# Performance work log

Hardware: AMD Instinct MI355X
Metric: run time of the kernel (lower is better)

The kernel has to match this reference:

```python
import jax, jax.numpy as jnp
import numpy as np


def setup_inputs() -> dict:
    key = jax.random.key(0)
    ks = jax.random.split(key, 5)
    B, Lq, Lkv, HQ, H, D, S, BS = 1, 256, 4096, 32, 2, 128, 16, 64
    q = jax.random.normal(ks[0], (B, Lq, HQ, D), jnp.float32)
    k = jax.random.normal(ks[1], (B, Lkv, H, D), jnp.float32)
    v = jax.random.normal(ks[2], (B, Lkv, H, D), jnp.float32)
    w = jax.random.uniform(ks[3], (B, Lq, HQ, S), jnp.float32)
    block_indices = jax.random.randint(ks[4], (B, Lq, H, S), 0, Lkv // BS).astype(jnp.int32)
    return {"q": q, "k": k, "v": v, "w": w, "block_indices": block_indices, "block_size": BS}


def reference(q, k, v, w, block_indices, block_size):
    # q: (B, Lq, HQ, D); k,v: (B, Lkv, H, D); w: (B, Lq, HQ, num_weights);
    # block_indices: (B, Lq, H, S) int32, entries < 0 are skipped.
    B, Lq, HQ, D = q.shape
    H = k.shape[2]
    S = block_indices.shape[-1]
    G = HQ // H  # query heads per kv head
    nb = k.shape[1] // block_size
    sm_scale = 1.0 / (D ** 0.5)  # default scale in the kernel

    # Reshape KV into blocks: (B, H, nb, BS, D)
    kb = k.reshape(B, nb, block_size, H, D).transpose(0, 3, 1, 2, 4)
    vb = v.reshape(B, nb, block_size, H, D).transpose(0, 3, 1, 2, 4)

    idx = block_indices.transpose(0, 2, 1, 3)  # (B, H, Lq, S)
    valid = idx >= 0
    idx = jnp.maximum(idx, 0)

    # Gather selected blocks per (batch, kv_head): -> (B, H, Lq, S, BS, D)
    gather = jax.vmap(jax.vmap(lambda blocks, ind: blocks[ind]))
    kg = gather(kb, idx)
    vg = gather(vb, idx)

    # Group query heads by kv head: (B, H, Lq, G, D)
    qh = q.reshape(B, Lq, H, G, D).transpose(0, 2, 1, 3, 4)

    # Per-block scores and per-block softmax over the BS keys (axis u)
    scores = jnp.einsum('bhlgd,bhlsud->bhlgsu', qh, kg) * sm_scale
    p = jax.nn.softmax(scores, axis=-1)

    # Per-(head, block) learned weight; only first S weights of w are used.
    wh = w[..., :S].reshape(B, Lq, H, G, S).transpose(0, 2, 1, 3, 4)  # (B,H,Lq,G,S)
    coef = wh * valid[:, :, :, None, :].astype(p.dtype)
    p = p * coef[..., None]

    o = jnp.einsum('bhlgsu,bhlsud->bhlgd', p, vg)  # (B, H, Lq, G, D)
    return o.transpose(0, 2, 1, 3, 4).reshape(B, Lq, HQ, D)
```

## Files before the change

kernel.cpp:

```cpp
#include <hip/hip_runtime.h>
#include <hip/hip_bf16.h>


namespace {

constexpr int kLq = 256, kHQ = 32, kH = 2, kG = 16, kD = 128, kS = 16;
constexpr int kNB = 64;
constexpr float kScaleLog2e = 0.08838834764831845f * 1.4426950408889634f;

constexpr int kKPackN = kH * kNB * 16 * 64;
constexpr int kPStr   = 72;
constexpr int kSStr   = 136;

constexpr int kQOff = 0;
constexpr int kPOff = 32768;

typedef short s16x8 __attribute__((ext_vector_type(8)));
typedef float f32x4 __attribute__((ext_vector_type(4)));

union U32BF2 { unsigned int u; __hip_bfloat162 h; };
union FragU  { uint4 u; s16x8 v; };

static __device__ inline unsigned int pk_bf16(float a, float b) {
    U32BF2 z; z.h = __float22bfloat162_rn(make_float2(a, b));
    return z.u;
}

__global__ __launch_bounds__(256)
void pack_kv(const float* __restrict__ k, const float* __restrict__ v,
             uint4* __restrict__ kp, uint4* __restrict__ vp)
{
    __shared__ unsigned short S_s[32 * kSStr];

    const int bid  = blockIdx.x;
    const int isV  = bid & 1;
    const int half = (bid >> 1) & 1;
    const int blk  = (bid >> 2) & 63;
    const int h    = bid >> 8;
    const int t    = threadIdx.x;
    const int lane = t & 63, n = lane & 15, quad = lane >> 4;
    const int wv   = t >> 6;

    {
        const float* src = (isV ? v : k) +
            ((size_t)(blk * 64 + half * 32) * kH + h) * kD;
        const int r0 = t >> 5, c4 = (t & 31) << 2;
        #pragma unroll
        for (int p = 0; p < 4; ++p) {
            const int r = p * 8 + r0;
            const float4 f = *(const float4*)(src + (size_t)r * (kH * kD) + c4);
            *(unsigned int*)&S_s[r * kSStr + c4]     = pk_bf16(f.x, f.y);
            *(unsigned int*)&S_s[r * kSStr + c4 + 2] = pk_bf16(f.z, f.w);
        }
    }
    __syncthreads();

    const size_t obase = (size_t)(h * 64 + blk) * 16 * 64;
    if (!isV) {
        #pragma unroll
        for (int rep = 0; rep < 2; ++rep) {
            const int cl    = wv * 2 + rep;
            const int t_loc = cl >> 2, st = cl & 3;
            const int c     = (2 * half + t_loc) * 4 + st;
            const int u_loc = t_loc * 16 + n;
            kp[obase + (size_t)c * 64 + lane] =
                *(const uint4*)&S_s[u_loc * kSStr + st * 32 + quad * 8];
        }
    } else {
        #pragma unroll
        for (int rep = 0; rep < 2; ++rep) {
            const int dt = wv * 2 + rep;
            const int c  = dt * 2 + half;
            const int d  = dt * 16 + n;
            unsigned short s[8];
            #pragma unroll
            for (int j = 0; j < 8; ++j) s[j] = S_s[(quad * 8 + j) * kSStr + d];
            uint4 val;
            val.x = s[0] | ((unsigned)s[1] << 16);
            val.y = s[2] | ((unsigned)s[3] << 16);
            val.z = s[4] | ((unsigned)s[5] << 16);
            val.w = s[6] | ((unsigned)s[7] << 16);
            vp[obase + (size_t)c * 64 + lane] = val;
        }
    }
}

__global__ __launch_bounds__(512, 4)
void hsa_main(const float* __restrict__ q, const float* __restrict__ w,
              const int* __restrict__ bidx, const uint4* __restrict__ kp,
              const uint4* __restrict__ vp, float* __restrict__ out)
{
    __shared__ __align__(16) unsigned char smem[69632];

    const int bid  = blockIdx.x;
    const int l    = bid >> 1;
    const int h    = bid & 1;
    const int tid  = threadIdx.x;
    const int wave = tid >> 6;
    const int lane = tid & 63;
    const int n    = lane & 15;
    const int quad = lane >> 4;

    unsigned char* qlds = smem + kQOff + wave * 4096 + lane * 16;
    {
        const float* qb = q + ((size_t)l * kHQ + h * kG + n) * kD + quad * 8;
        #pragma unroll
        for (int st = 0; st < 4; ++st) {
            const float4 f0 = *(const float4*)(qb + st * 32);
            const float4 f1 = *(const float4*)(qb + st * 32 + 4);
            uint4 z;
            z.x = pk_bf16(f0.x, f0.y); z.y = pk_bf16(f0.z, f0.w);
            z.z = pk_bf16(f1.x, f1.y); z.w = pk_bf16(f1.z, f1.w);
            *(uint4*)(qlds + st * 1024) = z;
        }
    }

    int   baseA, baseB;
    float wvalA, wvalB;
    {
        const int sA = wave * 2, sB = wave * 2 + 1;
        const int biA = bidx[(size_t)(l * kH + h) * kS + sA];
        const int biB = bidx[(size_t)(l * kH + h) * kS + sB];
        wvalA = (biA < 0) ? 0.f : w[((size_t)l * kHQ + h * kG + n) * kS + sA];
        wvalB = (biB < 0) ? 0.f : w[((size_t)l * kHQ + h * kG + n) * kS + sB];
        baseA = (h * kNB + max(biA, 0)) * 1024;
        baseB = (h * kNB + max(biB, 0)) * 1024;
    }

    unsigned short* PA = (unsigned short*)(smem + kPOff + wave * 4608);
    unsigned short* PB = PA + kG * kPStr;

    FragU kA[4], kB[4], vrA[4], vrB[4];
    #pragma unroll
    for (int st = 0; st < 4; ++st) kA[st].u = kp[baseA + st * 64 + lane];
    #pragma unroll
    for (int st = 0; st < 4; ++st) kB[st].u = kp[baseB + st * 64 + lane];
    #pragma unroll
    for (int i = 0; i < 4; ++i)    vrA[i].u = vp[baseA + i * 64 + lane];
    #pragma unroll
    for (int i = 0; i < 4; ++i)    vrB[i].u = vp[baseA + (4 + i) * 64 + lane];
    __builtin_amdgcn_sched_barrier(0);

    f32x4 oacc[8];
    #pragma unroll
    for (int dt = 0; dt < 8; ++dt) oacc[dt] = (f32x4){0.f, 0.f, 0.f, 0.f};

    float partA = 0.f, partB = 0.f;
    #pragma unroll
    for (int t = 0; t < 4; ++t) {
        {
            f32x4 sc = {0.f, 0.f, 0.f, 0.f};
            #pragma unroll
            for (int st = 0; st < 4; ++st) {
                const s16x8 aq = *(const s16x8*)(qlds + st * 1024);
                sc = __builtin_amdgcn_mfma_f32_16x16x32_bf16(kA[st].v, aq, sc, 0, 0, 0);
            }
            if (t < 3) {
                #pragma unroll
                for (int st = 0; st < 4; ++st)
                    kA[st].u = kp[baseA + ((t + 1) * 4 + st) * 64 + lane];
            }
            __builtin_amdgcn_sched_barrier(0);
            #pragma unroll
            for (int r = 0; r < 4; ++r) {
                sc[r] = exp2f(sc[r] * kScaleLog2e);
                partA += sc[r];
            }
            const unsigned long long pq =
                ((unsigned long long)pk_bf16(sc[2], sc[3]) << 32) | pk_bf16(sc[0], sc[1]);
            *(unsigned long long*)&PA[n * kPStr + t * 16 + quad * 4] = pq;
        }
        {
            f32x4 sc = {0.f, 0.f, 0.f, 0.f};
            #pragma unroll
            for (int st = 0; st < 4; ++st) {
                const s16x8 aq = *(const s16x8*)(qlds + st * 1024);
                sc = __builtin_amdgcn_mfma_f32_16x16x32_bf16(kB[st].v, aq, sc, 0, 0, 0);
            }
            if (t < 3) {
                #pragma unroll
                for (int st = 0; st < 4; ++st)
                    kB[st].u = kp[baseB + ((t + 1) * 4 + st) * 64 + lane];
            }
            __builtin_amdgcn_sched_barrier(0);
            #pragma unroll
            for (int r = 0; r < 4; ++r) {
                sc[r] = exp2f(sc[r] * kScaleLog2e);
                partB += sc[r];
            }
            const unsigned long long pq =
                ((unsigned long long)pk_bf16(sc[2], sc[3]) << 32) | pk_bf16(sc[0], sc[1]);
            *(unsigned long long*)&PB[n * kPStr + t * 16 + quad * 4] = pq;
        }
    }

    partA += __shfl_xor(partA, 16);
    partA += __shfl_xor(partA, 32);
    partB += __shfl_xor(partB, 16);
    partB += __shfl_xor(partB, 32);
    const float coefA = wvalA / partA;
    const float coefB = wvalB / partB;

    const f32x4 zero = {0.f, 0.f, 0.f, 0.f};

    {
        const s16x8 bf0 = *(const s16x8*)&PA[n * kPStr + quad * 8];
        const s16x8 bf1 = *(const s16x8*)&PA[n * kPStr + 32 + quad * 8];

        {
            f32x4 p0 = __builtin_amdgcn_mfma_f32_16x16x32_bf16(vrA[0].v, bf0, zero, 0, 0, 0);
            p0       = __builtin_amdgcn_mfma_f32_16x16x32_bf16(vrA[1].v, bf1, p0,   0, 0, 0);
            f32x4 p1 = __builtin_amdgcn_mfma_f32_16x16x32_bf16(vrA[2].v, bf0, zero, 0, 0, 0);
            p1       = __builtin_amdgcn_mfma_f32_16x16x32_bf16(vrA[3].v, bf1, p1,   0, 0, 0);
            #pragma unroll
            for (int i = 0; i < 4; ++i) vrA[i].u = vp[baseA + (8 + i) * 64 + lane];
            __builtin_amdgcn_sched_barrier(0);
            #pragma unroll
            for (int r = 0; r < 4; ++r) {
                oacc[0][r] = fmaf(coefA, p0[r], oacc[0][r]);
                oacc[1][r] = fmaf(coefA, p1[r], oacc[1][r]);
            }
        }
        {
            f32x4 p0 = __builtin_amdgcn_mfma_f32_16x16x32_bf16(vrB[0].v, bf0, zero, 0, 0, 0);
            p0       = __builtin_amdgcn_mfma_f32_16x16x32_bf16(vrB[1].v, bf1, p0,   0, 0, 0);
            f32x4 p1 = __builtin_amdgcn_mfma_f32_16x16x32_bf16(vrB[2].v, bf0, zero, 0, 0, 0);
            p1       = __builtin_amdgcn_mfma_f32_16x16x32_bf16(vrB[3].v, bf1, p1,   0, 0, 0);
            #pragma unroll
            for (int i = 0; i < 4; ++i) vrB[i].u = vp[baseA + (12 + i) * 64 + lane];
            __builtin_amdgcn_sched_barrier(0);
            #pragma unroll
            for (int r = 0; r < 4; ++r) {
                oacc[2][r] = fmaf(coefA, p0[r], oacc[2][r]);
                oacc[3][r] = fmaf(coefA, p1[r], oacc[3][r]);
            }
        }
        {
            f32x4 p0 = __builtin_amdgcn_mfma_f32_16x16x32_bf16(vrA[0].v, bf0, zero, 0, 0, 0);
            p0       = __builtin_amdgcn_mfma_f32_16x16x32_bf16(vrA[1].v, bf1, p0,   0, 0, 0);
            f32x4 p1 = __builtin_amdgcn_mfma_f32_16x16x32_bf16(vrA[2].v, bf0, zero, 0, 0, 0);
            p1       = __builtin_amdgcn_mfma_f32_16x16x32_bf16(vrA[3].v, bf1, p1,   0, 0, 0);
            #pragma unroll
            for (int i = 0; i < 4; ++i) vrA[i].u = vp[baseB + i * 64 + lane];
            __builtin_amdgcn_sched_barrier(0);
            #pragma unroll
            for (int r = 0; r < 4; ++r) {
                oacc[4][r] = fmaf(coefA, p0[r], oacc[4][r]);
                oacc[5][r] = fmaf(coefA, p1[r], oacc[5][r]);
            }
        }
        {
            f32x4 p0 = __builtin_amdgcn_mfma_f32_16x16x32_bf16(vrB[0].v, bf0, zero, 0, 0, 0);
            p0       = __builtin_amdgcn_mfma_f32_16x16x32_bf16(vrB[1].v, bf1, p0,   0, 0, 0);
            f32x4 p1 = __builtin_amdgcn_mfma_f32_16x16x32_bf16(vrB[2].v, bf0, zero, 0, 0, 0);
            p1       = __builtin_amdgcn_mfma_f32_16x16x32_bf16(vrB[3].v, bf1, p1,   0, 0, 0);
            #pragma unroll
            for (int i = 0; i < 4; ++i) vrB[i].u = vp[baseB + (4 + i) * 64 + lane];
            __builtin_amdgcn_sched_barrier(0);
            #pragma unroll
            for (int r = 0; r < 4; ++r) {
                oacc[6][r] = fmaf(coefA, p0[r], oacc[6][r]);
                oacc[7][r] = fmaf(coefA, p1[r], oacc[7][r]);
            }
        }
    }

    {
        const s16x8 bf0 = *(const s16x8*)&PB[n * kPStr + quad * 8];
        const s16x8 bf1 = *(const s16x8*)&PB[n * kPStr + 32 + quad * 8];

        {
            f32x4 p0 = __builtin_amdgcn_mfma_f32_16x16x32_bf16(vrA[0].v, bf0, zero, 0, 0, 0);
            p0       = __builtin_amdgcn_mfma_f32_16x16x32_bf16(vrA[1].v, bf1, p0,   0, 0, 0);
            f32x4 p1 = __builtin_amdgcn_mfma_f32_16x16x32_bf16(vrA[2].v, bf0, zero, 0, 0, 0);
            p1       = __builtin_amdgcn_mfma_f32_16x16x32_bf16(vrA[3].v, bf1, p1,   0, 0, 0);
            #pragma unroll
            for (int i = 0; i < 4; ++i) vrA[i].u = vp[baseB + (8 + i) * 64 + lane];
            __builtin_amdgcn_sched_barrier(0);
            #pragma unroll
            for (int r = 0; r < 4; ++r) {
                oacc[0][r] = fmaf(coefB, p0[r], oacc[0][r]);
                oacc[1][r] = fmaf(coefB, p1[r], oacc[1][r]);
            }
        }
        {
            f32x4 p0 = __builtin_amdgcn_mfma_f32_16x16x32_bf16(vrB[0].v, bf0, zero, 0, 0, 0);
            p0       = __builtin_amdgcn_mfma_f32_16x16x32_bf16(vrB[1].v, bf1, p0,   0, 0, 0);
            f32x4 p1 = __builtin_amdgcn_mfma_f32_16x16x32_bf16(vrB[2].v, bf0, zero, 0, 0, 0);
            p1       = __builtin_amdgcn_mfma_f32_16x16x32_bf16(vrB[3].v, bf1, p1,   0, 0, 0);
            #pragma unroll
            for (int i = 0; i < 4; ++i) vrB[i].u = vp[baseB + (12 + i) * 64 + lane];
            __builtin_amdgcn_sched_barrier(0);
            #pragma unroll
            for (int r = 0; r < 4; ++r) {
                oacc[2][r] = fmaf(coefB, p0[r], oacc[2][r]);
                oacc[3][r] = fmaf(coefB, p1[r], oacc[3][r]);
            }
        }
        {
            f32x4 p0 = __builtin_amdgcn_mfma_f32_16x16x32_bf16(vrA[0].v, bf0, zero, 0, 0, 0);
            p0       = __builtin_amdgcn_mfma_f32_16x16x32_bf16(vrA[1].v, bf1, p0,   0, 0, 0);
            f32x4 p1 = __builtin_amdgcn_mfma_f32_16x16x32_bf16(vrA[2].v, bf0, zero, 0, 0, 0);
            p1       = __builtin_amdgcn_mfma_f32_16x16x32_bf16(vrA[3].v, bf1, p1,   0, 0, 0);
            #pragma unroll
            for (int r = 0; r < 4; ++r) {
                oacc[4][r] = fmaf(coefB, p0[r], oacc[4][r]);
                oacc[5][r] = fmaf(coefB, p1[r], oacc[5][r]);
            }
        }
        {
            f32x4 p0 = __builtin_amdgcn_mfma_f32_16x16x32_bf16(vrB[0].v, bf0, zero, 0, 0, 0);
            p0       = __builtin_amdgcn_mfma_f32_16x16x32_bf16(vrB[1].v, bf1, p0,   0, 0, 0);
            f32x4 p1 = __builtin_amdgcn_mfma_f32_16x16x32_bf16(vrB[2].v, bf0, zero, 0, 0, 0);
            p1       = __builtin_amdgcn_mfma_f32_16x16x32_bf16(vrB[3].v, bf1, p1,   0, 0, 0);
            #pragma unroll
            for (int r = 0; r < 4; ++r) {
                oacc[6][r] = fmaf(coefB, p0[r], oacc[6][r]);
                oacc[7][r] = fmaf(coefB, p1[r], oacc[7][r]);
            }
        }
    }

    __syncthreads();
    float* epi = (float*)(smem + kQOff);

    if (wave >= 4) {
        #pragma unroll
        for (int dt = 0; dt < 8; ++dt)
            *(f32x4*)&epi[(wave - 4) * 2048 + dt * 256 + lane * 4] = oacc[dt];
    }
    __syncthreads();
    if (wave < 4) {
        #pragma unroll
        for (int dt = 0; dt < 8; ++dt) {
            const f32x4 o = *(const f32x4*)&epi[wave * 2048 + dt * 256 + lane * 4];
            #pragma unroll
            for (int r = 0; r < 4; ++r) oacc[dt][r] += o[r];
        }
    }
    __syncthreads();
    if (wave == 2 || wave == 3) {
        #pragma unroll
        for (int dt = 0; dt < 8; ++dt)
            *(f32x4*)&epi[(wave - 2) * 2048 + dt * 256 + lane * 4] = oacc[dt];
    }
    __syncthreads();
    if (wave < 2) {
        #pragma unroll
        for (int dt = 0; dt < 8; ++dt) {
            const f32x4 o = *(const f32x4*)&epi[wave * 2048 + dt * 256 + lane * 4];
            #pragma unroll
            for (int r = 0; r < 4; ++r) oacc[dt][r] += o[r];
        }
    }
    __syncthreads();
    if (wave == 1) {
        #pragma unroll
        for (int dt = 0; dt < 8; ++dt)
            *(f32x4*)&epi[dt * 256 + lane * 4] = oacc[dt];
    }
    __syncthreads();
    if (wave == 0) {
        float* ob = out + ((size_t)l * kHQ + h * kG + n) * kD;
        #pragma unroll
        for (int dt = 0; dt < 8; ++dt) {
            const f32x4 o = *(const f32x4*)&epi[dt * 256 + lane * 4];
            float4 val;
            #pragma unroll
            for (int r = 0; r < 4; ++r) (&val.x)[r] = oacc[dt][r] + o[r];
            *(float4*)(ob + dt * 16 + quad * 4) = val;
        }
    }
}

}

extern "C" void kernel_launch(void* const* d_in, const int* in_sizes, int n_in,
                              void* d_out, int out_size, void* d_ws, size_t ws_size,
                              hipStream_t stream)
{
    const float* q    = (const float*)d_in[0];
    const float* k    = (const float*)d_in[1];
    const float* v    = (const float*)d_in[2];
    const float* w    = (const float*)d_in[3];
    const int*   bidx = (const int*)d_in[4];
    float* out = (float*)d_out;

    uint4* kp = (uint4*)d_ws;
    uint4* vp = (uint4*)((char*)d_ws + (size_t)kKPackN * 16);

    pack_kv<<<dim3(512), dim3(256), 0, stream>>>(k, v, kp, vp);
    hsa_main<<<dim3(kLq * kH), dim3(512), 0, stream>>>(q, w, bidx, kp, vp, out);
}
```

Measured before the change: 88.82 us.

## Invert loop to iterate KV blocks with inverted index and separate reduction

The kernel is restructured from query-centric to KV-block-centric. A single-block kernel builds an inverted list of (query, slot) entries per KV block. The producer kernel then loads each K/V block once and reuses it across all queries that selected it, writing per-slot bf16 partial outputs to workspace. A reduction kernel sums those partials. Q is pre-packed to bf16 in its own kernel. This aims to cut redundant K/V gather traffic, but adds three launches, a serial single-block index build, a capped list size (512), and bf16 rounding of partial outputs before the sum.

```diff
diff --git a/kernel.cpp b/kernel.cpp
--- a/kernel.cpp
+++ b/kernel.cpp
@@ -11,9 +11,14 @@
 constexpr int kKPackN = kH * kNB * 16 * 64;
 constexpr int kPStr   = 72;
 constexpr int kSStr   = 136;
-
-constexpr int kQOff = 0;
-constexpr int kPOff = 32768;
+constexpr int kMaxE   = 512;
+
+constexpr size_t kOffKP   = 0;
+constexpr size_t kOffVP   = kOffKP + (size_t)kKPackN * 16;
+constexpr size_t kOffQP   = kOffVP + (size_t)kKPackN * 16;
+constexpr size_t kOffCnt  = kOffQP + (size_t)kLq * kH * 4 * 64 * 16;
+constexpr size_t kOffList = kOffCnt + 4096;
+constexpr size_t kOffWS   = kOffList + (size_t)kH * kNB * kMaxE * 4;
 
 typedef short s16x8 __attribute__((ext_vector_type(8)));
 typedef float f32x4 __attribute__((ext_vector_type(4)));
@@ -25,6 +30,14 @@
     U32BF2 z; z.h = __float22bfloat162_rn(make_float2(a, b));
     return z.u;
 }
+static __device__ inline float bf_lo(unsigned int u) {
+    return __uint_as_float(u << 16);
+}
+static __device__ inline float bf_hi(unsigned int u) {
+    return __uint_as_float(u & 0xffff0000u);
+}
+
+#define MF(a, b, c) __builtin_amdgcn_mfma_f32_16x16x32_bf16(a, b, c, 0, 0, 0)
 
 __global__ __launch_bounds__(256)
 void pack_kv(const float* __restrict__ k, const float* __restrict__ v,
@@ -85,292 +98,295 @@
     }
 }
 
+__global__ __launch_bounds__(256)
+void pack_q(const float* __restrict__ q, uint4* __restrict__ qp)
+{
+    const int l    = blockIdx.x;
+    const int t    = threadIdx.x;
+    const int lane = t & 63, n = lane & 15, quad = lane >> 4;
+    const int st   = t >> 6;
+    #pragma unroll
+    for (int h = 0; h < 2; ++h) {
+        const float* qb = q + ((size_t)l * kHQ + h * kG + n) * kD
+                            + st * 32 + quad * 8;
+        const float4 f0 = *(const float4*)qb;
+        const float4 f1 = *(const float4*)(qb + 4);
+        uint4 z;
+        z.x = pk_bf16(f0.x, f0.y); z.y = pk_bf16(f0.z, f0.w);
+        z.z = pk_bf16(f1.x, f1.y); z.w = pk_bf16(f1.z, f1.w);
+        qp[((size_t)(l * 2 + h) * 4 + st) * 64 + lane] = z;
+    }
+}
+
+__global__ __launch_bounds__(512)
+void build_index(const int* __restrict__ bidx, int* __restrict__ gcount,
+                 int* __restrict__ glist)
+{
+    __shared__ int cnt[kH * kNB];
+    const int t = threadIdx.x;
+    if (t < kH * kNB) cnt[t] = 0;
+    __syncthreads();
+    for (int id = t; id < kLq * kH * kS; id += 512) {
+        const int b = bidx[id];
+        if (b >= 0) {
+            const int l = id >> 5, h = (id >> 4) & 1, s = id & 15;
+            const int key = h * kNB + b;
+            const int pos = atomicAdd(&cnt[key], 1);
+            if (pos < kMaxE) glist[key * kMaxE + pos] = (l << 4) | s;
+        }
+    }
+    __syncthreads();
+    if (t < kH * kNB) gcount[t] = min(cnt[t], kMaxE);
+}
+
 __global__ __launch_bounds__(512, 4)
-void hsa_main(const float* __restrict__ q, const float* __restrict__ w,
-              const int* __restrict__ bidx, const uint4* __restrict__ kp,
-              const uint4* __restrict__ vp, float* __restrict__ out)
-{
-    __shared__ __align__(16) unsigned char smem[69632];
-
-    const int bid  = blockIdx.x;
-    const int l    = bid >> 1;
-    const int h    = bid & 1;
+void hsa_prod(const uint4* __restrict__ qp, const float* __restrict__ w,
+              const int* __restrict__ glist, const int* __restrict__ gcount,
+              const uint4* __restrict__ kp, const uint4* __restrict__ vp,
+              unsigned short* __restrict__ wsb)
+{
+    __shared__ __align__(16) unsigned char smem[36864];
+
+    const int p    = blockIdx.x;
+    const int h    = p >> 8;
+    const int b    = (p >> 2) & 63;
+    const int chunk= p & 3;
     const int tid  = threadIdx.x;
     const int wave = tid >> 6;
     const int lane = tid & 63;
     const int n    = lane & 15;
     const int quad = lane >> 4;
 
-    unsigned char* qlds = smem + kQOff + wave * 4096 + lane * 16;
-    {
-        const float* qb = q + ((size_t)l * kHQ + h * kG + n) * kD + quad * 8;
-        #pragma unroll
-        for (int st = 0; st < 4; ++st) {
-            const float4 f0 = *(const float4*)(qb + st * 32);
-            const float4 f1 = *(const float4*)(qb + st * 32 + 4);
-            uint4 z;
-            z.x = pk_bf16(f0.x, f0.y); z.y = pk_bf16(f0.z, f0.w);
-            z.z = pk_bf16(f1.x, f1.y); z.w = pk_bf16(f1.z, f1.w);
-            *(uint4*)(qlds + st * 1024) = z;
-        }
-    }
-
-    int   baseA, baseB;
-    float wvalA, wvalB;
-    {
-        const int sA = wave * 2, sB = wave * 2 + 1;
-        const int biA = bidx[(size_t)(l * kH + h) * kS + sA];
-        const int biB = bidx[(size_t)(l * kH + h) * kS + sB];
-        wvalA = (biA < 0) ? 0.f : w[((size_t)l * kHQ + h * kG + n) * kS + sA];
-        wvalB = (biB < 0) ? 0.f : w[((size_t)l * kHQ + h * kG + n) * kS + sB];
-        baseA = (h * kNB + max(biA, 0)) * 1024;
-        baseB = (h * kNB + max(biB, 0)) * 1024;
-    }
-
-    unsigned short* PA = (unsigned short*)(smem + kPOff + wave * 4608);
-    unsigned short* PB = PA + kG * kPStr;
-
-    FragU kA[4], kB[4], vrA[4], vrB[4];
+    const int count  = gcount[h * kNB + b];
+    const int baseKV = (h * kNB + b) * 1024;
+    const int lbase  = (h * kNB + b) * kMaxE;
+
+    unsigned short* PA = (unsigned short*)smem + wave * 2304;
+    unsigned short* PB = PA + 1152;
+
+    for (int j = 0; ; ++j) {
+        const int eA = chunk + 4 * (j * 16 + wave * 2);
+        if (eA >= count) break;
+        const int eB   = eA + 4;
+        const bool hasB = (eB < count);
+        const int entA = glist[lbase + eA];
+        const int entB = hasB ? glist[lbase + eB] : entA;
+        const int lA = entA >> 4, sA = entA & 15;
+        const int lB = entB >> 4, sB = entB & 15;
+        const float wvA = w[((size_t)lA * kHQ + h * kG + n) * kS + sA];
+        const float wvB = hasB ? w[((size_t)lB * kHQ + h * kG + n) * kS + sB] : 0.f;
+
+        FragU aqA[4], aqB[4], kk[4], vr0[4], vr1[4];
+        #pragma unroll
+        for (int st = 0; st < 4; ++st)
+            aqA[st].u = qp[((size_t)(lA * 2 + h) * 4 + st) * 64 + lane];
+        #pragma unroll
+        for (int st = 0; st < 4; ++st)
+            aqB[st].u = qp[((size_t)(lB * 2 + h) * 4 + st) * 64 + lane];
+        #pragma unroll
+        for (int st = 0; st < 4; ++st) kk[st].u = kp[baseKV + st * 64 + lane];
+        #pragma unroll
+        for (int i = 0; i < 4; ++i)    vr0[i].u = vp[baseKV + i * 64 + lane];
+        #pragma unroll
+        for (int i = 0; i < 4; ++i)    vr1[i].u = vp[baseKV + (4 + i) * 64 + lane];
+        __builtin_amdgcn_sched_barrier(0);
+
+        float partA = 0.f, partB = 0.f;
+        #pragma unroll
+        for (int t = 0; t < 4; ++t) {
+            f32x4 scA = {0.f, 0.f, 0.f, 0.f};
+            f32x4 scB = {0.f, 0.f, 0.f, 0.f};
+            #pragma unroll
+            for (int st = 0; st < 4; ++st) scA = MF(kk[st].v, aqA[st].v, scA);
+            #pragma unroll
+            for (int st = 0; st < 4; ++st) scB = MF(kk[st].v, aqB[st].v, scB);
+            if (t < 3) {
+                #pragma unroll
+                for (int st = 0; st < 4; ++st)
+                    kk[st].u = kp[baseKV + ((t + 1) * 4 + st) * 64 + lane];
+            }
+            __builtin_amdgcn_sched_barrier(0);
+            #pragma unroll
+            for (int r = 0; r < 4; ++r) {
+                scA[r] = exp2f(scA[r] * kScaleLog2e);
+                partA += scA[r];
+                scB[r] = exp2f(scB[r] * kScaleLog2e);
+                partB += scB[r];
+            }
+            *(unsigned long long*)&PA[n * kPStr + t * 16 + quad * 4] =
+                ((unsigned long long)pk_bf16(scA[2], scA[3]) << 32) |
+                pk_bf16(scA[0], scA[1]);
+            *(unsigned long long*)&PB[n * kPStr + t * 16 + quad * 4] =
+                ((unsigned long long)pk_bf16(scB[2], scB[3]) << 32) |
+                pk_bf16(scB[0], scB[1]);
+        }
+
+        partA += __shfl_xor(partA, 16);
+        partA += __shfl_xor(partA, 32);
+        partB += __shfl_xor(partB, 16);
+        partB += __shfl_xor(partB, 32);
+        const float coefA = wvA / partA;
+        const float coefB = wvB / partB;
+
+        const f32x4 zero = {0.f, 0.f, 0.f, 0.f};
+        f32x4 oacc[8];
+
+        {
+            const s16x8 bf0 = *(const s16x8*)&PA[n * kPStr + quad * 8];
+            const s16x8 bf1 = *(const s16x8*)&PA[n * kPStr + 32 + quad * 8];
+            {
+                f32x4 p0 = MF(vr0[0].v, bf0, zero); p0 = MF(vr0[1].v, bf1, p0);
+                f32x4 p1 = MF(vr0[2].v, bf0, zero); p1 = MF(vr0[3].v, bf1, p1);
+                #pragma unroll
+                for (int i = 0; i < 4; ++i) vr0[i].u = vp[baseKV + (8 + i) * 64 + lane];
+                __builtin_amdgcn_sched_barrier(0);
+                #pragma unroll
+                for (int r = 0; r < 4; ++r) {
+                    oacc[0][r] = coefA * p0[r];
+                    oacc[1][r] = coefA * p1[r];
+                }
+            }
+            {
+                f32x4 p0 = MF(vr1[0].v, bf0, zero); p0 = MF(vr1[1].v, bf1, p0);
+                f32x4 p1 = MF(vr1[2].v, bf0, zero); p1 = MF(vr1[3].v, bf1, p1);
+                #pragma unroll
+                for (int i = 0; i < 4; ++i) vr1[i].u = vp[baseKV + (12 + i) * 64 + lane];
+                __builtin_amdgcn_sched_barrier(0);
+                #pragma unroll
+                for (int r = 0; r < 4; ++r) {
+                    oacc[2][r] = coefA * p0[r];
+                    oacc[3][r] = coefA * p1[r];
+                }
+            }
+            {
+                f32x4 p0 = MF(vr0[0].v, bf0, zero); p0 = MF(vr0[1].v, bf1, p0);
+                f32x4 p1 = MF(vr0[2].v, bf0, zero); p1 = MF(vr0[3].v, bf1, p1);
+                #pragma unroll
+                for (int i = 0; i < 4; ++i) vr0[i].u = vp[baseKV + i * 64 + lane];
+                __builtin_amdgcn_sched_barrier(0);
+                #pragma unroll
+                for (int r = 0; r < 4; ++r) {
+                    oacc[4][r] = coefA * p0[r];
+                    oacc[5][r] = coefA * p1[r];
+                }
+            }
+            {
+                f32x4 p0 = MF(vr1[0].v, bf0, zero); p0 = MF(vr1[1].v, bf1, p0);
+                f32x4 p1 = MF(vr1[2].v, bf0, zero); p1 = MF(vr1[3].v, bf1, p1);
+                #pragma unroll
+                for (int i = 0; i < 4; ++i) vr1[i].u = vp[baseKV + (4 + i) * 64 + lane];
+                __builtin_amdgcn_sched_barrier(0);
+                #pragma unroll
+                for (int r = 0; r < 4; ++r) {
+                    oacc[6][r] = coefA * p0[r];
+                    oacc[7][r] = coefA * p1[r];
+                }
+            }
+        }
+        {
+            const size_t base = (((size_t)(lA * 2 + h) * 16 + sA) * 16 + n) * 128;
+            #pragma unroll
+            for (int dt = 0; dt < 8; ++dt) {
+                uint2 vv;
+                vv.x = pk_bf16(oacc[dt][0], oacc[dt][1]);
+                vv.y = pk_bf16(oacc[dt][2], oacc[dt][3]);
+                *(uint2*)(wsb + base + dt * 16 + quad * 4) = vv;
+            }
+        }
+
+        {
+            const s16x8 bf0 = *(const s16x8*)&PB[n * kPStr + quad * 8];
+            const s16x8 bf1 = *(const s16x8*)&PB[n * kPStr + 32 + quad * 8];
+            {
+                f32x4 p0 = MF(vr0[0].v, bf0, zero); p0 = MF(vr0[1].v, bf1, p0);
+                f32x4 p1 = MF(vr0[2].v, bf0, zero); p1 = MF(vr0[3].v, bf1, p1);
+                #pragma unroll
+                for (int i = 0; i < 4; ++i) vr0[i].u = vp[baseKV + (8 + i) * 64 + lane];
+                __builtin_amdgcn_sched_barrier(0);
+                #pragma unroll
+                for (int r = 0; r < 4; ++r) {
+                    oacc[0][r] = coefB * p0[r];
+                    oacc[1][r] = coefB * p1[r];
+                }
+            }
+            {
+                f32x4 p0 = MF(vr1[0].v, bf0, zero); p0 = MF(vr1[1].v, bf1, p0);
+                f32x4 p1 = MF(vr1[2].v, bf0, zero); p1 = MF(vr1[3].v, bf1, p1);
+                #pragma unroll
+                for (int i = 0; i < 4; ++i) vr1[i].u = vp[baseKV + (12 + i) * 64 + lane];
+                __builtin_amdgcn_sched_barrier(0);
+                #pragma unroll
+                for (int r = 0; r < 4; ++r) {
+                    oacc[2][r] = coefB * p0[r];
+                    oacc[3][r] = coefB * p1[r];
+                }
+            }
+            {
+                f32x4 p0 = MF(vr0[0].v, bf0, zero); p0 = MF(vr0[1].v, bf1, p0);
+                f32x4 p1 = MF(vr0[2].v, bf0, zero); p1 = MF(vr0[3].v, bf1, p1);
+                #pragma unroll
+                for (int r = 0; r < 4; ++r) {
+                    oacc[4][r] = coefB * p0[r];
+                    oacc[5][r] = coefB * p1[r];
+                }
+            }
+            {
+                f32x4 p0 = MF(vr1[0].v, bf0, zero); p0 = MF(vr1[1].v, bf1, p0);
+                f32x4 p1 = MF(vr1[2].v, bf0, zero); p1 = MF(vr1[3].v, bf1, p1);
+                #pragma unroll
+                for (int r = 0; r < 4; ++r) {
+                    oacc[6][r] = coefB * p0[r];
+                    oacc[7][r] = coefB * p1[r];
+                }
+            }
+        }
+        if (hasB) {
+            const size_t base = (((size_t)(lB * 2 + h) * 16 + sB) * 16 + n) * 128;
+            #pragma unroll
+            for (int dt = 0; dt < 8; ++dt) {
+                uint2 vv;
+                vv.x = pk_bf16(oacc[dt][0], oacc[dt][1]);
+                vv.y = pk_bf16(oacc[dt][2], oacc[dt][3]);
+                *(uint2*)(wsb + base + dt * 16 + quad * 4) = vv;
+            }
+        }
+    }
+}
+
+__global__ __launch_bounds__(256)
+void hsa_red(const unsigned short* __restrict__ wsb,
+             const int* __restrict__ bidx, float* __restrict__ out)
+{
+    const int p = blockIdx.x;
+    const int l = p >> 1, h = p & 1;
+    const int t = threadIdx.x;
+    const int g = t >> 4, dc = t & 15, d0 = dc * 8;
+
+    __shared__ int valid[16];
+    if (t < 16) valid[t] = bidx[(size_t)p * 16 + t];
+    __syncthreads();
+
+    float acc[8];
     #pragma unroll
-    for (int st = 0; st < 4; ++st) kA[st].u = kp[baseA + st * 64 + lane];
+    for (int r = 0; r < 8; ++r) acc[r] = 0.f;
+
     #pragma unroll
-    for (int st = 0; st < 4; ++st) kB[st].u = kp[baseB + st * 64 + lane];
-    #pragma unroll
-    for (int i = 0; i < 4; ++i)    vrA[i].u = vp[baseA + i * 64 + lane];
-    #pragma unroll
-    for (int i = 0; i < 4; ++i)    vrB[i].u = vp[baseA + (4 + i) * 64 + lane];
-    __builtin_amdgcn_sched_barrier(0);
-
-    f32x4 oacc[8];
-    #pragma unroll
-    for (int dt = 0; dt < 8; ++dt) oacc[dt] = (f32x4){0.f, 0.f, 0.f, 0.f};
-
-    float partA = 0.f, partB = 0.f;
-    #pragma unroll
-    for (int t = 0; t < 4; ++t) {
-        {
-            f32x4 sc = {0.f, 0.f, 0.f, 0.f};
-            #pragma unroll
-            for (int st = 0; st < 4; ++st) {
-                const s16x8 aq = *(const s16x8*)(qlds + st * 1024);
-                sc = __builtin_amdgcn_mfma_f32_16x16x32_bf16(kA[st].v, aq, sc, 0, 0, 0);
-            }
-            if (t < 3) {
-                #pragma unroll
-                for (int st = 0; st < 4; ++st)
-                    kA[st].u = kp[baseA + ((t + 1) * 4 + st) * 64 + lane];
-            }
-            __builtin_amdgcn_sched_barrier(0);
-            #pragma unroll
-            for (int r = 0; r < 4; ++r) {
-                sc[r] = exp2f(sc[r] * kScaleLog2e);
-                partA += sc[r];
-            }
-            const unsigned long long pq =
-                ((unsigned long long)pk_bf16(sc[2], sc[3]) << 32) | pk_bf16(sc[0], sc[1]);
-            *(unsigned long long*)&PA[n * kPStr + t * 16 + quad * 4] = pq;
-        }
-        {
-            f32x4 sc = {0.f, 0.f, 0.f, 0.f};
-            #pragma unroll
-            for (int st = 0; st < 4; ++st) {
-                const s16x8 aq = *(const s16x8*)(qlds + st * 1024);
-                sc = __builtin_amdgcn_mfma_f32_16x16x32_bf16(kB[st].v, aq, sc, 0, 0, 0);
-            }
-            if (t < 3) {
-                #pragma unroll
-                for (int st = 0; st < 4; ++st)
-                    kB[st].u = kp[baseB + ((t + 1) * 4 + st) * 64 + lane];
-            }
-            __builtin_amdgcn_sched_barrier(0);
-            #pragma unroll
-            for (int r = 0; r < 4; ++r) {
-                sc[r] = exp2f(sc[r] * kScaleLog2e);
-                partB += sc[r];
-            }
-            const unsigned long long pq =
-                ((unsigned long long)pk_bf16(sc[2], sc[3]) << 32) | pk_bf16(sc[0], sc[1]);
-            *(unsigned long long*)&PB[n * kPStr + t * 16 + quad * 4] = pq;
-        }
-    }
-
-    partA += __shfl_xor(partA, 16);
-    partA += __shfl_xor(partA, 32);
-    partB += __shfl_xor(partB, 16);
-    partB += __shfl_xor(partB, 32);
-    const float coefA = wvalA / partA;
-    const float coefB = wvalB / partB;
-
-    const f32x4 zero = {0.f, 0.f, 0.f, 0.f};
-
-    {
-        const s16x8 bf0 = *(const s16x8*)&PA[n * kPStr + quad * 8];
-        const s16x8 bf1 = *(const s16x8*)&PA[n * kPStr + 32 + quad * 8];
-
-        {
-            f32x4 p0 = __builtin_amdgcn_mfma_f32_16x16x32_bf16(vrA[0].v, bf0, zero, 0, 0, 0);
-            p0       = __builtin_amdgcn_mfma_f32_16x16x32_bf16(vrA[1].v, bf1, p0,   0, 0, 0);
-            f32x4 p1 = __builtin_amdgcn_mfma_f32_16x16x32_bf16(vrA[2].v, bf0, zero, 0, 0, 0);
-            p1       = __builtin_amdgcn_mfma_f32_16x16x32_bf16(vrA[3].v, bf1, p1,   0, 0, 0);
-            #pragma unroll
-            for (int i = 0; i < 4; ++i) vrA[i].u = vp[baseA + (8 + i) * 64 + lane];
-            __builtin_amdgcn_sched_barrier(0);
-            #pragma unroll
-            for (int r = 0; r < 4; ++r) {
-                oacc[0][r] = fmaf(coefA, p0[r], oacc[0][r]);
-                oacc[1][r] = fmaf(coefA, p1[r], oacc[1][r]);
-            }
-        }
-        {
-            f32x4 p0 = __builtin_amdgcn_mfma_f32_16x16x32_bf16(vrB[0].v, bf0, zero, 0, 0, 0);
-            p0       = __builtin_amdgcn_mfma_f32_16x16x32_bf16(vrB[1].v, bf1, p0,   0, 0, 0);
-            f32x4 p1 = __builtin_amdgcn_mfma_f32_16x16x32_bf16(vrB[2].v, bf0, zero, 0, 0, 0);
-            p1       = __builtin_amdgcn_mfma_f32_16x16x32_bf16(vrB[3].v, bf1, p1,   0, 0, 0);
-            #pragma unroll
-            for (int i = 0; i < 4; ++i) vrB[i].u = vp[baseA + (12 + i) * 64 + lane];
-            __builtin_amdgcn_sched_barrier(0);
-            #pragma unroll
-            for (int r = 0; r < 4; ++r) {
-                oacc[2][r] = fmaf(coefA, p0[r], oacc[2][r]);
-                oacc[3][r] = fmaf(coefA, p1[r], oacc[3][r]);
-            }
-        }
-        {
-            f32x4 p0 = __builtin_amdgcn_mfma_f32_16x16x32_bf16(vrA[0].v, bf0, zero, 0, 0, 0);
-            p0       = __builtin_amdgcn_mfma_f32_16x16x32_bf16(vrA[1].v, bf1, p0,   0, 0, 0);
-            f32x4 p1 = __builtin_amdgcn_mfma_f32_16x16x32_bf16(vrA[2].v, bf0, zero, 0, 0, 0);
-            p1       = __builtin_amdgcn_mfma_f32_16x16x32_bf16(vrA[3].v, bf1, p1,   0, 0, 0);
-            #pragma unroll
-            for (int i = 0; i < 4; ++i) vrA[i].u = vp[baseB + i * 64 + lane];
-            __builtin_amdgcn_sched_barrier(0);
-            #pragma unroll
-            for (int r = 0; r < 4; ++r) {
-                oacc[4][r] = fmaf(coefA, p0[r], oacc[4][r]);
-                oacc[5][r] = fmaf(coefA, p1[r], oacc[5][r]);
-            }
-        }
-        {
-            f32x4 p0 = __builtin_amdgcn_mfma_f32_16x16x32_bf16(vrB[0].v, bf0, zero, 0, 0, 0);
-            p0       = __builtin_amdgcn_mfma_f32_16x16x32_bf16(vrB[1].v, bf1, p0,   0, 0, 0);
-            f32x4 p1 = __builtin_amdgcn_mfma_f32_16x16x32_bf16(vrB[2].v, bf0, zero, 0, 0, 0);
-            p1       = __builtin_amdgcn_mfma_f32_16x16x32_bf16(vrB[3].v, bf1, p1,   0, 0, 0);
-            #pragma unroll
-            for (int i = 0; i < 4; ++i) vrB[i].u = vp[baseB + (4 + i) * 64 + lane];
-            __builtin_amdgcn_sched_barrier(0);
-            #pragma unroll
-            for (int r = 0; r < 4; ++r) {
-                oacc[6][r] = fmaf(coefA, p0[r], oacc[6][r]);
-                oacc[7][r] = fmaf(coefA, p1[r], oacc[7][r]);
-            }
-        }
-    }
-
-    {
-        const s16x8 bf0 = *(const s16x8*)&PB[n * kPStr + quad * 8];
-        const s16x8 bf1 = *(const s16x8*)&PB[n * kPStr + 32 + quad * 8];
-
-        {
-            f32x4 p0 = __builtin_amdgcn_mfma_f32_16x16x32_bf16(vrA[0].v, bf0, zero, 0, 0, 0);
-            p0       = __builtin_amdgcn_mfma_f32_16x16x32_bf16(vrA[1].v, bf1, p0,   0, 0, 0);
-            f32x4 p1 = __builtin_amdgcn_mfma_f32_16x16x32_bf16(vrA[2].v, bf0, zero, 0, 0, 0);
-            p1       = __builtin_amdgcn_mfma_f32_16x16x32_bf16(vrA[3].v, bf1, p1,   0, 0, 0);
-            #pragma unroll
-            for (int i = 0; i < 4; ++i) vrA[i].u = vp[baseB + (8 + i) * 64 + lane];
-            __builtin_amdgcn_sched_barrier(0);
-            #pragma unroll
-            for (int r = 0; r < 4; ++r) {
-                oacc[0][r] = fmaf(coefB, p0[r], oacc[0][r]);
-                oacc[1][r] = fmaf(coefB, p1[r], oacc[1][r]);
-            }
-        }
-        {
-            f32x4 p0 = __builtin_amdgcn_mfma_f32_16x16x32_bf16(vrB[0].v, bf0, zero, 0, 0, 0);
-            p0       = __builtin_amdgcn_mfma_f32_16x16x32_bf16(vrB[1].v, bf1, p0,   0, 0, 0);
-            f32x4 p1 = __builtin_amdgcn_mfma_f32_16x16x32_bf16(vrB[2].v, bf0, zero, 0, 0, 0);
-            p1       = __builtin_amdgcn_mfma_f32_16x16x32_bf16(vrB[3].v, bf1, p1,   0, 0, 0);
-            #pragma unroll
-            for (int i = 0; i < 4; ++i) vrB[i].u = vp[baseB + (12 + i) * 64 + lane];
-            __builtin_amdgcn_sched_barrier(0);
-            #pragma unroll
-            for (int r = 0; r < 4; ++r) {
-                oacc[2][r] = fmaf(coefB, p0[r], oacc[2][r]);
-                oacc[3][r] = fmaf(coefB, p1[r], oacc[3][r]);
-            }
-        }
-        {
-            f32x4 p0 = __builtin_amdgcn_mfma_f32_16x16x32_bf16(vrA[0].v, bf0, zero, 0, 0, 0);
-            p0       = __builtin_amdgcn_mfma_f32_16x16x32_bf16(vrA[1].v, bf1, p0,   0, 0, 0);
-            f32x4 p1 = __builtin_amdgcn_mfma_f32_16x16x32_bf16(vrA[2].v, bf0, zero, 0, 0, 0);
-            p1       = __builtin_amdgcn_mfma_f32_16x16x32_bf16(vrA[3].v, bf1, p1,   0, 0, 0);
-            #pragma unroll
-            for (int r = 0; r < 4; ++r) {
-                oacc[4][r] = fmaf(coefB, p0[r], oacc[4][r]);
-                oacc[5][r] = fmaf(coefB, p1[r], oacc[5][r]);
-            }
-        }
-        {
-            f32x4 p0 = __builtin_amdgcn_mfma_f32_16x16x32_bf16(vrB[0].v, bf0, zero, 0, 0, 0);
-            p0       = __builtin_amdgcn_mfma_f32_16x16x32_bf16(vrB[1].v, bf1, p0,   0, 0, 0);
-            f32x4 p1 = __builtin_amdgcn_mfma_f32_16x16x32_bf16(vrB[2].v, bf0, zero, 0, 0, 0);
-            p1       = __builtin_amdgcn_mfma_f32_16x16x32_bf16(vrB[3].v, bf1, p1,   0, 0, 0);
-            #pragma unroll
-            for (int r = 0; r < 4; ++r) {
-                oacc[6][r] = fmaf(coefB, p0[r], oacc[6][r]);
-                oacc[7][r] = fmaf(coefB, p1[r], oacc[7][r]);
-            }
-        }
-    }
-
-    __syncthreads();
-    float* epi = (float*)(smem + kQOff);
-
-    if (wave >= 4) {
-        #pragma unroll
-        for (int dt = 0; dt < 8; ++dt)
-            *(f32x4*)&epi[(wave - 4) * 2048 + dt * 256 + lane * 4] = oacc[dt];
-    }
-    __syncthreads();
-    if (wave < 4) {
-        #pragma unroll
-        for (int dt = 0; dt < 8; ++dt) {
-            const f32x4 o = *(const f32x4*)&epi[wave * 2048 + dt * 256 + lane * 4];
-            #pragma unroll
-            for (int r = 0; r < 4; ++r) oacc[dt][r] += o[r];
-        }
-    }
-    __syncthreads();
-    if (wave == 2 || wave == 3) {
-        #pragma unroll
-        for (int dt = 0; dt < 8; ++dt)
-            *(f32x4*)&epi[(wave - 2) * 2048 + dt * 256 + lane * 4] = oacc[dt];
-    }
-    __syncthreads();
-    if (wave < 2) {
-        #pragma unroll
-        for (int dt = 0; dt < 8; ++dt) {
-            const f32x4 o = *(const f32x4*)&epi[wave * 2048 + dt * 256 + lane * 4];
-            #pragma unroll
-            for (int r = 0; r < 4; ++r) oacc[dt][r] += o[r];
-        }
-    }
-    __syncthreads();
-    if (wave == 1) {
-        #pragma unroll
-        for (int dt = 0; dt < 8; ++dt)
-            *(f32x4*)&epi[dt * 256 + lane * 4] = oacc[dt];
-    }
-    __syncthreads();
-    if (wave == 0) {
-        float* ob = out + ((size_t)l * kHQ + h * kG + n) * kD;
-        #pragma unroll
-        for (int dt = 0; dt < 8; ++dt) {
-            const f32x4 o = *(const f32x4*)&epi[dt * 256 + lane * 4];
-            float4 val;
-            #pragma unroll
-            for (int r = 0; r < 4; ++r) (&val.x)[r] = oacc[dt][r] + o[r];
-            *(float4*)(ob + dt * 16 + quad * 4) = val;
-        }
-    }
+    for (int s = 0; s < 16; ++s) {
+        if (valid[s] < 0) continue;
+        const uint4 vv = *(const uint4*)(wsb +
+            (((size_t)p * 16 + s) * 16 + g) * 128 + d0);
+        acc[0] += bf_lo(vv.x); acc[1] += bf_hi(vv.x);
+        acc[2] += bf_lo(vv.y); acc[3] += bf_hi(vv.y);
+        acc[4] += bf_lo(vv.z); acc[5] += bf_hi(vv.z);
+        acc[6] += bf_lo(vv.w); acc[7] += bf_hi(vv.w);
+    }
+
+    float* ob = out + ((size_t)l * kHQ + h * kG + g) * kD + d0;
+    float4 o0, o1;
+    o0.x = acc[0]; o0.y = acc[1]; o0.z = acc[2]; o0.w = acc[3];
+    o1.x = acc[4]; o1.y = acc[5]; o1.z = acc[6]; o1.w = acc[7];
+    *(float4*)ob       = o0;
+    *(float4*)(ob + 4) = o1;
 }
 
 }
@@ -386,9 +402,17 @@
     const int*   bidx = (const int*)d_in[4];
     float* out = (float*)d_out;
 
-    uint4* kp = (uint4*)d_ws;
-    uint4* vp = (uint4*)((char*)d_ws + (size_t)kKPackN * 16);
+    char* ws = (char*)d_ws;
+    uint4*          kp     = (uint4*)(ws + kOffKP);
+    uint4*          vp     = (uint4*)(ws + kOffVP);
+    uint4*          qp     = (uint4*)(ws + kOffQP);
+    int*            gcount = (int*)(ws + kOffCnt);
+    int*            glist  = (int*)(ws + kOffList);
+    unsigned short* wsb    = (unsigned short*)(ws + kOffWS);
 
     pack_kv<<<dim3(512), dim3(256), 0, stream>>>(k, v, kp, vp);
-    hsa_main<<<dim3(kLq * kH), dim3(512), 0, stream>>>(q, w, bidx, kp, vp, out);
-}
+    pack_q<<<dim3(256), dim3(256), 0, stream>>>(q, qp);
+    build_index<<<dim3(1), dim3(512), 0, stream>>>(bidx, gcount, glist);
+    hsa_prod<<<dim3(512), dim3(512), 0, stream>>>(qp, w, glist, gcount, kp, vp, wsb);
+    hsa_red<<<dim3(512), dim3(256), 0, stream>>>(wsb, bidx, out);
+}
```

Result: slower. 145.1 us (+63.3%).
